# Performance work log

Hardware: AMD Instinct MI355X
Metric: run time of the kernel (lower is better)

## Reference

```python
import jax, jax.numpy as jnp
import numpy as np

RANK = 8
ALPHA = 16.0
SCALING = ALPHA / RANK  # 2.0
B, S, DIN, DOUT = 4, 4096, 4096, 4096


def setup_inputs() -> dict:
    key = jax.random.key(0)
    k = jax.random.split(key, 6)
    return {
        "x": jax.random.normal(k[0], (B, S, DIN), dtype=jnp.float32),
        "codes": jax.random.normal(k[1], (B, S, RANK), dtype=jnp.float32),
        "W": jax.random.normal(k[2], (DOUT, DIN), dtype=jnp.float32) * 0.02,
        "b": jax.random.normal(k[3], (DOUT,), dtype=jnp.float32) * 0.02,
        "lora_U": jax.random.normal(k[4], (DOUT, RANK), dtype=jnp.float32) * 0.02,
        "lora_V": jax.random.normal(k[5], (DIN, RANK), dtype=jnp.float32) * 0.02,
    }


def reference(x, codes, W, b, lora_U, lora_V):
    # base linear: x @ W^T + b  -> [B, S, DOUT]
    base = jnp.einsum("bsi,oi->bso", x, W) + b
    # generated low-rank update: (x @ V) gated by per-token codes, then @ U^T
    xv = jnp.einsum("bsi,ir->bsr", x, lora_V)          # [B, S, rank]
    lora = jnp.einsum("bsr,or->bso", xv * codes, lora_U)  # [B, S, DOUT]
    return base + lora * SCALING
```

## Files before the change

kernel.cpp:

```cpp
#include <hip/hip_runtime.h>
#include <hip/hip_bf16.h>


typedef __bf16 bf16_t;
typedef __bf16 bf16x8 __attribute__((ext_vector_type(8)));
typedef float f32x4 __attribute__((ext_vector_type(4)));

#define M_TOT 16384
#define N_TOT 4096
#define K_TOT 4096
#define NT 64

#define GLOAD_LDS16(gp, lp)                                                    \
  __builtin_amdgcn_global_load_lds(                                            \
      (const __attribute__((address_space(1))) void*)(gp),                     \
      (__attribute__((address_space(3))) void*)(lp), 16, 0, 0)

__global__ void __launch_bounds__(256) prep_fused_kernel(
    const float* __restrict__ x, const float* __restrict__ codes,
    const float* __restrict__ V, const float* __restrict__ W,
    bf16_t* __restrict__ xbf, bf16_t* __restrict__ wbf,
    float* __restrict__ g) {
  const int tid = threadIdx.x;
  if (blockIdx.x >= 4096) {
    size_t i = ((size_t)(blockIdx.x - 4096) * 256 + tid) * 8;
    const float4* p = (const float4*)(W + i);
    float4 a = p[0], b = p[1];
    bf16x8 v;
    v[0] = (bf16_t)a.x; v[1] = (bf16_t)a.y; v[2] = (bf16_t)a.z; v[3] = (bf16_t)a.w;
    v[4] = (bf16_t)b.x; v[5] = (bf16_t)b.y; v[6] = (bf16_t)b.z; v[7] = (bf16_t)b.w;
    *(bf16x8*)(wbf + i) = v;
    return;
  }
  const int lane = tid & 63;
  const int wv = tid >> 6;
  const int m0 = blockIdx.x * 4;
  const int c0 = tid * 16;

  float xv[4][8];
#pragma unroll
  for (int rr = 0; rr < 4; ++rr)
#pragma unroll
    for (int r = 0; r < 8; ++r) xv[rr][r] = 0.f;

#pragma unroll
  for (int h = 0; h < 2; ++h) {
    const int cb = c0 + h * 8;
    float xr[4][8];
#pragma unroll
    for (int rr = 0; rr < 4; ++rr) {
      const float4* xp = (const float4*)(x + (size_t)(m0 + rr) * K_TOT + cb);
      float4 a0 = xp[0], a1 = xp[1];
      xr[rr][0] = a0.x; xr[rr][1] = a0.y; xr[rr][2] = a0.z; xr[rr][3] = a0.w;
      xr[rr][4] = a1.x; xr[rr][5] = a1.y; xr[rr][6] = a1.z; xr[rr][7] = a1.w;
      bf16x8 bv;
#pragma unroll
      for (int t = 0; t < 8; ++t) bv[t] = (bf16_t)xr[rr][t];
      *(bf16x8*)(xbf + (size_t)(m0 + rr) * K_TOT + cb) = bv;
    }
#pragma unroll
    for (int t = 0; t < 8; ++t) {
      const float4* vp = (const float4*)(V + (size_t)(cb + t) * 8);
      float4 v0 = vp[0], v1 = vp[1];
#pragma unroll
      for (int rr = 0; rr < 4; ++rr) {
        float xi = xr[rr][t];
        xv[rr][0] += xi * v0.x; xv[rr][1] += xi * v0.y;
        xv[rr][2] += xi * v0.z; xv[rr][3] += xi * v0.w;
        xv[rr][4] += xi * v1.x; xv[rr][5] += xi * v1.y;
        xv[rr][6] += xi * v1.z; xv[rr][7] += xi * v1.w;
      }
    }
  }

  __shared__ float red[4][4][8];
#pragma unroll
  for (int rr = 0; rr < 4; ++rr)
#pragma unroll
    for (int r = 0; r < 8; ++r) {
      float v = xv[rr][r];
      for (int s = 32; s > 0; s >>= 1) v += __shfl_down(v, s);
      if (lane == 0) red[wv][rr][r] = v;
    }
  __syncthreads();
  if (tid < 32) {
    int rr = tid >> 3, r = tid & 7;
    float tot = red[0][rr][r] + red[1][rr][r] + red[2][rr][r] + red[3][rr][r];
    int m = m0 + rr;
    g[m * 8 + r] = tot * codes[(size_t)m * 8 + r] * 2.0f;
  }
}

#define BAR __builtin_amdgcn_s_barrier()
#define VMC4 asm volatile("s_waitcnt vmcnt(4)" ::: "memory")
#define VMC0 asm volatile("s_waitcnt vmcnt(0)" ::: "memory")

#define STAGE(DB, AB, HALF, KT, SRC)                                           \
  {                                                                            \
    _Pragma("unroll") for (int r_ = 0; r_ < 2; ++r_) {                         \
      int rowl_ = (HALF) * 128 + (r_ * 8 + w) * 8 + srow;                      \
      const bf16_t* gp_ = (SRC) + (size_t)rowl_ * K_TOT + (KT) * 64 + sgk;     \
      GLOAD_LDS16(gp_, &lds[(DB) * 2 + (AB)][rowl_ * 64 + sj * 8]);            \
    }                                                                          \
  }

#define READ_A(BUF, MI0, DST)                                                  \
  _Pragma("unroll") for (int mi_ = 0; mi_ < 4; ++mi_) {                        \
    DST[mi_][0] = *(const bf16x8*)&lds[(BUF) * 2][arow0 + ((MI0) + mi_) * 1024 + aslot0]; \
    DST[mi_][1] = *(const bf16x8*)&lds[(BUF) * 2][arow0 + ((MI0) + mi_) * 1024 + aslot1]; \
  }

#define READ_B(BUF, NJ0, DST)                                                  \
  _Pragma("unroll") for (int nj_ = 0; nj_ < 2; ++nj_) {                        \
    DST[nj_][0] = *(const bf16x8*)&lds[(BUF) * 2 + 1][brow0 + ((NJ0) + nj_) * 1024 + aslot0]; \
    DST[nj_][1] = *(const bf16x8*)&lds[(BUF) * 2 + 1][brow0 + ((NJ0) + nj_) * 1024 + aslot1]; \
  }

#define MFMA_Q(MI0, NJ0, ASRC, BSRC)                                           \
  __builtin_amdgcn_s_setprio(1);                                               \
  _Pragma("unroll") for (int mi_ = 0; mi_ < 4; ++mi_)                          \
  _Pragma("unroll") for (int nj_ = 0; nj_ < 2; ++nj_) {                        \
    acc[(MI0) + mi_][(NJ0) + nj_] = __builtin_amdgcn_mfma_f32_16x16x32_bf16(   \
        ASRC[mi_][0], BSRC[nj_][0], acc[(MI0) + mi_][(NJ0) + nj_], 0, 0, 0);   \
    acc[(MI0) + mi_][(NJ0) + nj_] = __builtin_amdgcn_mfma_f32_16x16x32_bf16(   \
        ASRC[mi_][1], BSRC[nj_][1], acc[(MI0) + mi_][(NJ0) + nj_], 0, 0, 0);   \
  }                                                                            \
  __builtin_amdgcn_s_setprio(0);

#define KTILE(BUF, KT, S1, S2, VM)                                             \
  if (S1) STAGE(BUF ^ 1, 0, 1, (KT) + 1, aSrc);                                \
  if ((VM) == 4) { VMC4; } else { VMC0; }                                      \
  BAR;                                                                         \
  READ_A(BUF, 0, aF);                                                          \
  READ_B(BUF, 0, b01);                                                         \
  MFMA_Q(0, 0, aF, b01);                                                       \
  READ_B(BUF, 2, b23);                                                         \
  BAR;                                                                         \
  if (S1) STAGE(BUF ^ 1, 1, 0, (KT) + 1, bSrc);                                \
  MFMA_Q(0, 2, aF, b23);                                                       \
  READ_A(BUF, 4, aG);                                                          \
  BAR;                                                                         \
  if (S1) STAGE(BUF ^ 1, 1, 1, (KT) + 1, bSrc);                                \
  MFMA_Q(4, 2, aG, b23);                                                       \
  BAR;                                                                         \
  if (S2) STAGE(BUF, 0, 0, (KT) + 2, aSrc);                                    \
  MFMA_Q(4, 0, aG, b01);                                                       \
  BAR;

__global__ void __launch_bounds__(512) gemm_kernel(
    const bf16_t* __restrict__ A,
    const bf16_t* __restrict__ Bm,
    const float* __restrict__ bias, const float* __restrict__ U,
    const float* __restrict__ g, float* __restrict__ out) {
  const int tid = threadIdx.x;
  const int lane = tid & 63;
  const int w = tid >> 6;
  const int wr = w >> 2;
  const int wc = w & 3;
  const int llo = lane & 15, lhi = lane >> 4;

  int bid = blockIdx.x;
  int sw = (bid & 7) * 128 + (bid >> 3);
  const int bm = sw >> 4;
  const int bn = sw & 15;

  __shared__ __attribute__((aligned(128))) bf16_t lds[4][16384];

  const bf16_t* aSrc = A + (size_t)bm * 256 * K_TOT;
  const bf16_t* bSrc = Bm + (size_t)bn * 256 * K_TOT;

  const int srow = lane >> 3;
  const int sj = lane & 7;
  const int sgk = (sj ^ srow) * 8;

  const int xs = llo & 7;
  const int arow0 = (wr * 128 + llo) * 64;
  const int brow0 = (wc * 64 + llo) * 64;
  const int aslot0 = ((0 + lhi) ^ xs) * 8;
  const int aslot1 = ((4 + lhi) ^ xs) * 8;

  f32x4 acc[8][4] = {};
  bf16x8 aF[4][2], aG[4][2], b01[2][2], b23[2][2];

  STAGE(0, 0, 0, 0, aSrc);
  STAGE(0, 0, 1, 0, aSrc);
  STAGE(0, 1, 0, 0, bSrc);
  STAGE(0, 1, 1, 0, bSrc);
  STAGE(1, 0, 0, 1, aSrc);

#pragma unroll 1
  for (int t = 0; t < NT - 2; t += 2) {
    KTILE(0, t, 1, 1, 4);
    KTILE(1, t + 1, 1, 1, 4);
  }
  KTILE(0, NT - 2, 1, 0, 4);
  KTILE(1, NT - 1, 0, 0, 0);

  const int n0 = bn * 256 + wc * 64;
  int nidx[4];
  float biasv[4];
  float Un[4][8];
#pragma unroll
  for (int nj = 0; nj < 4; ++nj) {
    int n = n0 + nj * 16 + llo;
    nidx[nj] = n;
    biasv[nj] = bias[n];
    const float4* up = (const float4*)(U + (size_t)n * 8);
    float4 u0 = up[0], u1 = up[1];
    Un[nj][0] = u0.x; Un[nj][1] = u0.y; Un[nj][2] = u0.z; Un[nj][3] = u0.w;
    Un[nj][4] = u1.x; Un[nj][5] = u1.y; Un[nj][6] = u1.z; Un[nj][7] = u1.w;
  }
#pragma unroll
  for (int mi = 0; mi < 8; ++mi) {
#pragma unroll
    for (int reg = 0; reg < 4; ++reg) {
      int m = bm * 256 + wr * 128 + mi * 16 + lhi * 4 + reg;
      const float4* gp = (const float4*)(g + m * 8);
      float4 g0 = gp[0], g1 = gp[1];
      float* orow = out + (size_t)m * N_TOT;
#pragma unroll
      for (int nj = 0; nj < 4; ++nj) {
        float lora = g0.x * Un[nj][0] + g0.y * Un[nj][1] + g0.z * Un[nj][2] +
                     g0.w * Un[nj][3] + g1.x * Un[nj][4] + g1.y * Un[nj][5] +
                     g1.z * Un[nj][6] + g1.w * Un[nj][7];
        orow[nidx[nj]] = acc[mi][nj][reg] + biasv[nj] + lora;
      }
    }
  }
}

__global__ void __launch_bounds__(256) naive_kernel(
    const float* __restrict__ x, const float* __restrict__ codes,
    const float* __restrict__ W, const float* __restrict__ bias,
    const float* __restrict__ U, const float* __restrict__ V,
    float* __restrict__ out) {
  int m = blockIdx.x >> 4;
  int n = ((blockIdx.x & 15) << 8) + threadIdx.x;
  const float* xr = x + (size_t)m * K_TOT;
  const float* wrow = W + (size_t)n * K_TOT;
  float acc = 0.f;
  float xv[8] = {0, 0, 0, 0, 0, 0, 0, 0};
  for (int k = 0; k < K_TOT; k += 4) {
    float4 xa = *(const float4*)(xr + k);
    float4 wa = *(const float4*)(wrow + k);
    acc += xa.x * wa.x + xa.y * wa.y + xa.z * wa.z + xa.w * wa.w;
    const float* xs = (const float*)&xa;
#pragma unroll
    for (int t = 0; t < 4; ++t) {
      const float* vrow = V + (size_t)(k + t) * 8;
      float xi = xs[t];
#pragma unroll
      for (int r = 0; r < 8; ++r) xv[r] += xi * vrow[r];
    }
  }
  float lora = 0.f;
#pragma unroll
  for (int r = 0; r < 8; ++r)
    lora += xv[r] * codes[(size_t)m * 8 + r] * U[(size_t)n * 8 + r];
  out[(size_t)m * N_TOT + n] = acc + bias[n] + 2.0f * lora;
}

extern "C" void kernel_launch(void* const* d_in, const int* in_sizes, int n_in,
                              void* d_out, int out_size, void* d_ws,
                              size_t ws_size, hipStream_t stream) {
  const float* x = (const float*)d_in[0];
  const float* codes = (const float*)d_in[1];
  const float* W = (const float*)d_in[2];
  const float* b = (const float*)d_in[3];
  const float* U = (const float*)d_in[4];
  const float* V = (const float*)d_in[5];
  float* out = (float*)d_out;

  const size_t xbf_bytes = (size_t)M_TOT * K_TOT * 2;
  const size_t wbf_bytes = (size_t)N_TOT * K_TOT * 2;
  const size_t g_bytes = (size_t)M_TOT * 8 * 4;

  if (ws_size >= xbf_bytes + wbf_bytes + g_bytes) {
    bf16_t* xbf = (bf16_t*)d_ws;
    bf16_t* wbf = (bf16_t*)((char*)d_ws + xbf_bytes);
    float* g = (float*)((char*)d_ws + xbf_bytes + wbf_bytes);
    hipLaunchKernelGGL(prep_fused_kernel, dim3(12288), dim3(256), 0, stream,
                       x, codes, V, W, xbf, wbf, g);
    hipLaunchKernelGGL(gemm_kernel, dim3(1024), dim3(512), 0, stream, xbf, wbf,
                       b, U, g, out);
  } else {
    hipLaunchKernelGGL(naive_kernel, dim3((M_TOT) * (N_TOT / 256)), dim3(256),
                       0, stream, x, codes, W, b, U, V, out);
  }
}
```

Measured before the change: 606.6 us.

## Shrink GEMM K-tile to 32 with simple double-buffered pipeline

Changes the bf16 GEMM main loop from 64-wide K tiles with a multi-phase interleaved schedule to 32-wide K tiles. Each tile is loaded into a double buffer and then consumed by a single block of MFMAs. LDS usage halves, the swizzle is adapted to 32-element rows, and the staging/read/compute interleaving is simplified to one barrier pair per tile. The loop now runs twice as many iterations with more barriers per unit of work and less overlap between loads and MFMAs, in exchange for a simpler schedule and lower LDS footprint.

```diff
diff --git a/kernel.cpp b/kernel.cpp
--- a/kernel.cpp
+++ b/kernel.cpp
@@ -9,7 +9,7 @@
 #define M_TOT 16384
 #define N_TOT 4096
 #define K_TOT 4096
-#define NT 64
+#define NT32 128
 
 #define GLOAD_LDS16(gp, lp)                                                    \
   __builtin_amdgcn_global_load_lds(                                            \
@@ -95,56 +95,32 @@
 #define VMC4 asm volatile("s_waitcnt vmcnt(4)" ::: "memory")
 #define VMC0 asm volatile("s_waitcnt vmcnt(0)" ::: "memory")
 
-#define STAGE(DB, AB, HALF, KT, SRC)                                           \
+#define STAGE32(DB, AB, KT, SRC)                                               \
   {                                                                            \
-    _Pragma("unroll") for (int r_ = 0; r_ < 2; ++r_) {                         \
-      int rowl_ = (HALF) * 128 + (r_ * 8 + w) * 8 + srow;                      \
-      const bf16_t* gp_ = (SRC) + (size_t)rowl_ * K_TOT + (KT) * 64 + sgk;     \
-      GLOAD_LDS16(gp_, &lds[(DB) * 2 + (AB)][rowl_ * 64 + sj * 8]);            \
+    _Pragma("unroll") for (int i_ = 0; i_ < 2; ++i_) {                         \
+      int row_ = i_ * 128 + w * 16 + (lane >> 2);                              \
+      const bf16_t* gp_ = (SRC) + (size_t)row_ * K_TOT + (KT) * 32 + sgk32;    \
+      GLOAD_LDS16(gp_, &lds[(DB) * 2 + (AB)][(i_ * 512 + w * 64 + lane) * 8]); \
     }                                                                          \
   }
 
-#define READ_A(BUF, MI0, DST)                                                  \
-  _Pragma("unroll") for (int mi_ = 0; mi_ < 4; ++mi_) {                        \
-    DST[mi_][0] = *(const bf16x8*)&lds[(BUF) * 2][arow0 + ((MI0) + mi_) * 1024 + aslot0]; \
-    DST[mi_][1] = *(const bf16x8*)&lds[(BUF) * 2][arow0 + ((MI0) + mi_) * 1024 + aslot1]; \
-  }
-
-#define READ_B(BUF, NJ0, DST)                                                  \
-  _Pragma("unroll") for (int nj_ = 0; nj_ < 2; ++nj_) {                        \
-    DST[nj_][0] = *(const bf16x8*)&lds[(BUF) * 2 + 1][brow0 + ((NJ0) + nj_) * 1024 + aslot0]; \
-    DST[nj_][1] = *(const bf16x8*)&lds[(BUF) * 2 + 1][brow0 + ((NJ0) + nj_) * 1024 + aslot1]; \
-  }
-
-#define MFMA_Q(MI0, NJ0, ASRC, BSRC)                                           \
+#define KT32(BUF, KT, S)                                                       \
+  if (S) {                                                                     \
+    STAGE32(BUF ^ 1, 0, (KT) + 1, aSrc);                                       \
+    STAGE32(BUF ^ 1, 1, (KT) + 1, bSrc);                                       \
+  }                                                                            \
+  if (S) { VMC4; } else { VMC0; }                                              \
+  BAR;                                                                         \
+  _Pragma("unroll") for (int mi_ = 0; mi_ < 8; ++mi_)                          \
+      aR[mi_] = *(const bf16x8*)&lds[(BUF) * 2][aoff + mi_ * 512];             \
+  _Pragma("unroll") for (int nj_ = 0; nj_ < 4; ++nj_)                          \
+      bR[nj_] = *(const bf16x8*)&lds[(BUF) * 2 + 1][boff + nj_ * 512];         \
   __builtin_amdgcn_s_setprio(1);                                               \
-  _Pragma("unroll") for (int mi_ = 0; mi_ < 4; ++mi_)                          \
-  _Pragma("unroll") for (int nj_ = 0; nj_ < 2; ++nj_) {                        \
-    acc[(MI0) + mi_][(NJ0) + nj_] = __builtin_amdgcn_mfma_f32_16x16x32_bf16(   \
-        ASRC[mi_][0], BSRC[nj_][0], acc[(MI0) + mi_][(NJ0) + nj_], 0, 0, 0);   \
-    acc[(MI0) + mi_][(NJ0) + nj_] = __builtin_amdgcn_mfma_f32_16x16x32_bf16(   \
-        ASRC[mi_][1], BSRC[nj_][1], acc[(MI0) + mi_][(NJ0) + nj_], 0, 0, 0);   \
-  }                                                                            \
-  __builtin_amdgcn_s_setprio(0);
-
-#define KTILE(BUF, KT, S1, S2, VM)                                             \
-  if (S1) STAGE(BUF ^ 1, 0, 1, (KT) + 1, aSrc);                                \
-  if ((VM) == 4) { VMC4; } else { VMC0; }                                      \
-  BAR;                                                                         \
-  READ_A(BUF, 0, aF);                                                          \
-  READ_B(BUF, 0, b01);                                                         \
-  MFMA_Q(0, 0, aF, b01);                                                       \
-  READ_B(BUF, 2, b23);                                                         \
-  BAR;                                                                         \
-  if (S1) STAGE(BUF ^ 1, 1, 0, (KT) + 1, bSrc);                                \
-  MFMA_Q(0, 2, aF, b23);                                                       \
-  READ_A(BUF, 4, aG);                                                          \
-  BAR;                                                                         \
-  if (S1) STAGE(BUF ^ 1, 1, 1, (KT) + 1, bSrc);                                \
-  MFMA_Q(4, 2, aG, b23);                                                       \
-  BAR;                                                                         \
-  if (S2) STAGE(BUF, 0, 0, (KT) + 2, aSrc);                                    \
-  MFMA_Q(4, 0, aG, b01);                                                       \
+  _Pragma("unroll") for (int mi_ = 0; mi_ < 8; ++mi_)                          \
+  _Pragma("unroll") for (int nj_ = 0; nj_ < 4; ++nj_)                          \
+      acc[mi_][nj_] = __builtin_amdgcn_mfma_f32_16x16x32_bf16(                 \
+          aR[mi_], bR[nj_], acc[mi_][nj_], 0, 0, 0);                           \
+  __builtin_amdgcn_s_setprio(0);                                               \
   BAR;
 
 __global__ void __launch_bounds__(512) gemm_kernel(
@@ -164,37 +140,30 @@
   const int bm = sw >> 4;
   const int bn = sw & 15;
 
-  __shared__ __attribute__((aligned(128))) bf16_t lds[4][16384];
+  __shared__ __attribute__((aligned(128))) bf16_t lds[4][8192];
 
   const bf16_t* aSrc = A + (size_t)bm * 256 * K_TOT;
   const bf16_t* bSrc = Bm + (size_t)bn * 256 * K_TOT;
 
-  const int srow = lane >> 3;
-  const int sj = lane & 7;
-  const int sgk = (sj ^ srow) * 8;
-
-  const int xs = llo & 7;
-  const int arow0 = (wr * 128 + llo) * 64;
-  const int brow0 = (wc * 64 + llo) * 64;
-  const int aslot0 = ((0 + lhi) ^ xs) * 8;
-  const int aslot1 = ((4 + lhi) ^ xs) * 8;
+  const int sgk32 = ((lane & 3) ^ ((lane >> 3) & 3)) * 8;
+
+  const int rslot = (lhi ^ ((llo >> 1) & 3)) * 8;
+  const int aoff = (wr * 128 + llo) * 32 + rslot;
+  const int boff = (wc * 64 + llo) * 32 + rslot;
 
   f32x4 acc[8][4] = {};
-  bf16x8 aF[4][2], aG[4][2], b01[2][2], b23[2][2];
-
-  STAGE(0, 0, 0, 0, aSrc);
-  STAGE(0, 0, 1, 0, aSrc);
-  STAGE(0, 1, 0, 0, bSrc);
-  STAGE(0, 1, 1, 0, bSrc);
-  STAGE(1, 0, 0, 1, aSrc);
+  bf16x8 aR[8], bR[4];
+
+  STAGE32(0, 0, 0, aSrc);
+  STAGE32(0, 1, 0, bSrc);
 
 #pragma unroll 1
-  for (int t = 0; t < NT - 2; t += 2) {
-    KTILE(0, t, 1, 1, 4);
-    KTILE(1, t + 1, 1, 1, 4);
-  }
-  KTILE(0, NT - 2, 1, 0, 4);
-  KTILE(1, NT - 1, 0, 0, 0);
+  for (int t = 0; t < NT32 - 2; t += 2) {
+    KT32(0, t, 1);
+    KT32(1, t + 1, 1);
+  }
+  KT32(0, NT32 - 2, 1);
+  KT32(1, NT32 - 1, 0);
 
   const int n0 = bn * 256 + wc * 64;
   int nidx[4];
```

Result: slower. 684.4 us (+12.8%).
